# Performance work log

Measured on AMD Instinct MI355X. Metric: run time of the kernel, lower is better.

Reference implementation:

```python
import jax, jax.numpy as jnp
import numpy as np

KAPPA = 0.1          # temperature for sinkhorn routing
SINK_ITERS = 3
SINK_EPS = 1e-6
NORM_EPS = 1e-12     # F.normalize clamp
LOG_EPS = 2.220446049250313e-16  # np.finfo(float).eps
K_TOP = 1


def _l2norm(v, axis=-1):
    n = jnp.sqrt(jnp.sum(v * v, axis=axis, keepdims=True))
    return v / jnp.maximum(n, NORM_EPS)


def _sinkhorn(log_alpha):
    # log_alpha: [K, N]
    L = jnp.exp(log_alpha)
    for _ in range(SINK_ITERS):
        L = L / (jnp.sum(L, axis=1, keepdims=True) + SINK_EPS)
        L = L / (jnp.sum(L, axis=0, keepdims=True) + SINK_EPS)
    return L


def setup_inputs() -> dict:
    key = jax.random.key(0)
    ks = jax.random.split(key, 16)
    dim = 1024
    N = 32768
    lora_dim = [8, 16, 32, 48, 64, 96, 128]
    inp = {
        "x": jax.random.normal(ks[0], (N, dim), dtype=jnp.float32),
        "prototypes": jax.random.normal(ks[1], (7, dim), dtype=jnp.float32),
    }
    for e, d in enumerate(lora_dim):
        # torch Linear weight: [out_features, in_features]
        inp[f"A{e}"] = jax.random.normal(ks[2 + 2 * e], (d, dim), dtype=jnp.float32) * (1.0 / np.sqrt(dim))
        inp[f"B{e}"] = jax.random.normal(ks[3 + 2 * e], (dim, d), dtype=jnp.float32) * (1.0 / np.sqrt(d))
    return inp


def reference(x, prototypes, A0, B0, A1, B1, A2, B2, A3, B3, A4, B4, A5, B5, A6, B6):
    A = [A0, A1, A2, A3, A4, A5, A6]
    B = [B0, B1, B2, B3, B4, B5, B6]
    N = x.shape[0]
    num_experts = len(A)

    # --- sinkhorn routing: gates [N, K] ---
    x_n = _l2norm(x)                       # [N, D]
    p_n = _l2norm(prototypes)              # [K, D]
    sim = jnp.einsum('kd,nd->kn', p_n, x_n)  # [K, N]
    L = _sinkhorn(sim / KAPPA)             # [K, N] doubly-stochastic-ish
    gates_full = L.T                       # [N, K]

    # --- top-k sparsification (k=1) ---
    top_vals, top_idx = jax.lax.top_k(gates_full, K_TOP)  # [N, k]
    gates = jnp.zeros_like(gates_full).at[jnp.arange(N)[:, None], top_idx].set(top_vals)

    # --- per-expert LoRA + weighted log-space combine ---
    # combine: out[b] = log( sum_e gates[b,e] * exp(B_e(A_e(x_b))) ), eps floor
    combined = jnp.zeros_like(x)
    for e in range(num_experts):
        y = jnp.einsum('nr,dr->nd', jnp.einsum('nd,rd->nr', x, A[e]), B[e])  # [N, D]
        combined = combined + gates[:, e:e + 1] * jnp.exp(y)
    combined = jnp.where(combined == 0, LOG_EPS, combined)
    return jnp.log(combined)
```

## Files before the change

### kernel.cpp

```cpp
#include <hip/hip_runtime.h>
#include <math.h>

#define NTOK 32768
#define DIM  1024
#define NE   7
#define TROW 448

#define PN_OFF   0
#define R1_OFF   7168
#define R2_OFF   7176
#define R3_OFF   7184
#define CNT_OFF  7192
#define PR1_OFF  7200
#define PR2_OFF  23584
#define PR3_OFF  24608
#define E0_OFF   25632
#define LG_OFF   287776
#define LIST_OFF 320544
#define A16_OFF  549920
#define B16_OFF  754720
#define TALL_OFF_BYTES 3936384
#define NBLK 2055

#define SEPS 1e-6f

typedef __attribute__((ext_vector_type(8))) short short8v;
typedef __attribute__((ext_vector_type(4))) float f32x4;

constexpr int DV[7]   = {8, 16, 32, 48, 64, 96, 128};
constexpr int DPV[7]  = {32, 32, 32, 64, 64, 96, 128};
constexpr int DAPV[7] = {16, 16, 32, 48, 64, 96, 128};
constexpr int AOV[7]  = {0, 16384, 32768, 65536, 114688, 180224, 278528};
constexpr int BOV[7]  = {0, 32768, 65536, 98304, 163840, 229376, 327680};
constexpr int APRE[7] = {0, 32, 64, 96, 160, 224, 320};
constexpr int TCOL[25] = {0, 32, 64, 80, 96, 112, 128, 160, 176, 192, 208,
                          224, 240, 256, 272, 288, 304,
                          320, 336, 352, 368, 384, 400, 416, 432};

struct ExpPtrs { const float* A[NE]; const float* B[NE]; };

__device__ __forceinline__ short f2bf(float f) {
  union { float f; unsigned u; } v; v.f = f;
  return (short)((v.u + 0x7FFFu + ((v.u >> 16) & 1u)) >> 16);
}

__device__ __forceinline__ float wsum(float v) {
  #pragma unroll
  for (int off = 32; off > 0; off >>= 1) v += __shfl_xor(v, off);
  return v;
}

__device__ __forceinline__ float dot4acc(float4 a, float4 b, float acc) {
  acc = fmaf(a.x, b.x, acc);
  acc = fmaf(a.y, b.y, acc);
  acc = fmaf(a.z, b.z, acc);
  acc = fmaf(a.w, b.w, acc);
  return acc;
}

__device__ __forceinline__ void ecfg(int e, int& d, int& dp, int& dap, int& ao, int& bo) {
  switch (e) {
    case 0: d = 8;   dp = 32;  dap = 16;  ao = 0;      bo = 0;      break;
    case 1: d = 16;  dp = 32;  dap = 16;  ao = 16384;  bo = 32768;  break;
    case 2: d = 32;  dp = 32;  dap = 32;  ao = 32768;  bo = 65536;  break;
    case 3: d = 48;  dp = 64;  dap = 48;  ao = 65536;  bo = 98304;  break;
    case 4: d = 64;  dp = 64;  dap = 64;  ao = 114688; bo = 163840; break;
    case 5: d = 96;  dp = 96;  dap = 96;  ao = 180224; bo = 229376; break;
    default: d = 128; dp = 128; dap = 128; ao = 278528; bo = 327680; break;
  }
}

__global__ __launch_bounds__(256) void k_conv(ExpPtrs p, short* __restrict__ A16,
                                              short* __restrict__ B16,
                                              const float* __restrict__ proto,
                                              float* __restrict__ wsf,
                                              int* __restrict__ counts) {
  const int e = blockIdx.y;
  const int tid = threadIdx.x;
  int d, dp, dap, ao, bo;
  ecfg(e, d, dp, dap, ao, bo);

  if (blockIdx.x == 0) {
    __shared__ float pred[4];
    if (e == 0 && tid < 8) counts[tid] = 0;
    const int w = tid >> 6, lane = tid & 63;
    float v4[4], ss = 0.f;
    #pragma unroll
    for (int i = 0; i < 4; ++i) {
      v4[i] = proto[e * DIM + tid + 256 * i];
      ss = fmaf(v4[i], v4[i], ss);
    }
    ss = wsum(ss);
    if (lane == 0) pred[w] = ss;
    __syncthreads();
    float tot = ((pred[0] + pred[1]) + pred[2]) + pred[3];
    float inv = 1.f / fmaxf(sqrtf(tot), 1e-12f);
    #pragma unroll
    for (int i = 0; i < 4; ++i)
      wsf[PN_OFF + e * DIM + tid + 256 * i] = v4[i] * inv;
  }

  const float* A = p.A[e];
  const float* B = p.B[e];
  short* Ad = A16 + ao;
  short* Bd = B16 + bo;
  const int t0 = blockIdx.x * 256 + tid;
  for (int i = t0; i < dap * DIM; i += 16 * 256) {
    int row = i >> 10;
    Ad[i] = (row < d) ? f2bf(A[i]) : (short)0;
  }
  for (int i = t0; i < DIM * dp; i += 16 * 256) {
    int j = i / dp, r = i - j * dp;
    Bd[i] = (r < d) ? f2bf(B[j * d + r]) : (short)0;
  }
}

__global__ __launch_bounds__(512, 4) void k_simT(const float* __restrict__ x,
                                                 const short* __restrict__ A16,
                                                 const float* __restrict__ wsf,
                                                 float* __restrict__ e0,
                                                 float* __restrict__ pr1,
                                                 short* __restrict__ Tall) {
  __shared__ __align__(16) short As[400 * 40];
  __shared__ float pnS[7][32];
  __shared__ float prS[4][16][8];
  const int tid = threadIdx.x;
  const int n0 = blockIdx.x * 64;

  for (int i = tid; i < 64 * 48; i += 512) {
    int r = i / 48, c = i - r * 48;
    int col = (c < 16) ? (16 + c) : ((c < 32) ? (32 + c) : (112 + c));
    Tall[(size_t)(n0 + r) * TROW + col] = 0;
  }

  const int w = tid >> 6, lane = tid & 63, lo = lane & 15, hi = lane >> 4;
  const int mh = w >> 1, nh = w & 1;
  const int tokBase = n0 + mh * 16;
  const int ts = nh * 12;
  const float* xp = x + (size_t)(tokBase + lo) * DIM + hi * 8;
  const float* PN = wsf + PN_OFF;

  f32x4 acc[13];
  #pragma unroll
  for (int t = 0; t < 13; ++t) acc[t] = (f32x4){0.f, 0.f, 0.f, 0.f};
  float dk[7] = {0.f, 0.f, 0.f, 0.f, 0.f, 0.f, 0.f};
  float xx = 0.f;

  for (int kc = 0; kc < DIM; kc += 32) {
    for (int i = tid; i < 1600; i += 512) {
      int r = i >> 2, q = i & 3;
      *(short8v*)&As[r * 40 + q * 8] =
          *(const short8v*)(A16 + (size_t)r * DIM + kc + q * 8);
    }
    if (tid < 224) pnS[tid >> 5][tid & 31] = PN[(tid >> 5) * DIM + kc + (tid & 31)];
    __syncthreads();

    float4 x0 = *(const float4*)(xp + kc);
    float4 x1 = *(const float4*)(xp + kc + 4);
    short8v af;
    af[0] = f2bf(x0.x); af[1] = f2bf(x0.y); af[2] = f2bf(x0.z); af[3] = f2bf(x0.w);
    af[4] = f2bf(x1.x); af[5] = f2bf(x1.y); af[6] = f2bf(x1.z); af[7] = f2bf(x1.w);

    if (nh == 0) {
      xx = dot4acc(x0, x0, dot4acc(x1, x1, xx));
      #pragma unroll
      for (int k = 0; k < 7; ++k) {
        float4 p0 = *(const float4*)&pnS[k][hi * 8];
        float4 p1 = *(const float4*)&pnS[k][hi * 8 + 4];
        dk[k] = dot4acc(x0, p0, dot4acc(x1, p1, dk[k]));
      }
    }
    #pragma unroll
    for (int tt = 0; tt < 13; ++tt) {
      short8v bf = *(const short8v*)&As[(16 * (ts + tt) + lo) * 40 + hi * 8];
      acc[tt] = __builtin_amdgcn_mfma_f32_16x16x32_bf16(af, bf, acc[tt], 0, 0, 0);
    }
    __syncthreads();
  }

  const int tw = 12 + nh;
  #pragma unroll
  for (int tt = 0; tt < 13; ++tt) {
    if (tt < tw) {
      int col = TCOL[ts + tt] + lo;
      #pragma unroll
      for (int j = 0; j < 4; ++j)
        Tall[(size_t)(tokBase + hi * 4 + j) * TROW + col] = f2bf(acc[tt][j]);
    }
  }

  if (nh == 0) {
    #pragma unroll
    for (int k = 0; k < 7; ++k) {
      dk[k] += __shfl_xor(dk[k], 16);
      dk[k] += __shfl_xor(dk[k], 32);
    }
    xx += __shfl_xor(xx, 16);
    xx += __shfl_xor(xx, 32);
    if (hi == 0) {
      float nrm = fmaxf(sqrtf(xx), 1e-12f);
      int n = tokBase + lo;
      #pragma unroll
      for (int k = 0; k < 7; ++k) {
        float ev = expf((dk[k] / nrm) / 0.1f);
        e0[(size_t)n * 8 + k] = ev;
        prS[mh][lo][k] = ev;
      }
      prS[mh][lo][7] = 0.f;
    }
  }
  __syncthreads();
  if (tid < 8) {
    float s = 0.f;
    for (int m2 = 0; m2 < 4; ++m2)
      for (int l2 = 0; l2 < 16; ++l2) s += prS[m2][l2][tid];
    pr1[blockIdx.x * 8 + tid] = s;
  }
}

#define SUM7(l) (((((((l)[0] + (l)[1]) + (l)[2]) + (l)[3]) + (l)[4]) + (l)[5]) + (l)[6])

template<int DEPTH>
__global__ __launch_bounds__(256) void k_pass(const float* __restrict__ e0,
                                              float* __restrict__ wsf,
                                              const float* __restrict__ src, int nb,
                                              float* __restrict__ prOut,
                                              int* __restrict__ counts,
                                              int* __restrict__ list,
                                              float* __restrict__ lgv) {
  __shared__ float red2[8][33];
  __shared__ float Rcur[8];
  const int tid = threadIdx.x;
  {
    const int k = tid & 7, m = tid >> 3;
    float a = 0.f;
    for (int b = m; b < nb; b += 32) a += src[b * 8 + k];
    red2[k][m] = a;
    __syncthreads();
    if (tid < 8) {
      float s = 0.f;
      for (int mm = 0; mm < 32; ++mm) s += red2[tid][mm];
      Rcur[tid] = s;
      if (blockIdx.x == 0) {
        int roff = (DEPTH == 1) ? R1_OFF : (DEPTH == 2) ? R2_OFF : R3_OFF;
        wsf[roff + tid] = s;
      }
    }
    __syncthreads();
  }

  const int n = blockIdx.x * 256 + tid;
  float4 v0 = *(const float4*)(e0 + (size_t)n * 8);
  float4 v1 = *(const float4*)(e0 + (size_t)n * 8 + 4);
  float l[NE] = {v0.x, v0.y, v0.z, v0.w, v1.x, v1.y, v1.z};
  {
    const float* R1 = (DEPTH == 1) ? Rcur : (wsf + R1_OFF);
    #pragma unroll
    for (int k = 0; k < NE; ++k) l[k] = l[k] / (R1[k] + SEPS);
    float C = SUM7(l);
    #pragma unroll
    for (int k = 0; k < NE; ++k) l[k] = l[k] / (C + SEPS);
  }
  if constexpr (DEPTH >= 2) {
    const float* R2 = (DEPTH == 2) ? Rcur : (wsf + R2_OFF);
    #pragma unroll
    for (int k = 0; k < NE; ++k) l[k] = l[k] / (R2[k] + SEPS);
    float C = SUM7(l);
    #pragma unroll
    for (int k = 0; k < NE; ++k) l[k] = l[k] / (C + SEPS);
  }
  if constexpr (DEPTH >= 3) {
    const float* R3 = Rcur;
    #pragma unroll
    for (int k = 0; k < NE; ++k) l[k] = l[k] / (R3[k] + SEPS);
    float C = SUM7(l);
    #pragma unroll
    for (int k = 0; k < NE; ++k) l[k] = l[k] / (C + SEPS);
  }
  if constexpr (DEPTH == 3) {
    float best = l[0]; int be = 0;
    #pragma unroll
    for (int k = 1; k < NE; ++k) {
      if (l[k] > best) { best = l[k]; be = k; }
    }
    __shared__ int lcnt[8];
    __shared__ int wbase[4][8];
    __shared__ int gbase[8];
    const int w = tid >> 6, lane = tid & 63;
    if (tid < 8) lcnt[tid] = 0;
    __syncthreads();
    int rank = 0;
    #pragma unroll
    for (int k = 0; k < NE; ++k) {
      unsigned long long m = __ballot(be == k);
      if (lane == 0) wbase[w][k] = m ? atomicAdd(&lcnt[k], (int)__popcll(m)) : 0;
      if (be == k) rank = (int)__popcll(m & ((1ull << lane) - 1ull));
    }
    __syncthreads();
    if (tid < 8) gbase[tid] = lcnt[tid] ? atomicAdd(&counts[tid], lcnt[tid]) : 0;
    __syncthreads();
    int pos = gbase[be] + wbase[w][be] + rank;
    list[be * NTOK + pos] = n;
    lgv[n] = logf(best);
  } else {
    __shared__ float red[NE][256];
    #pragma unroll
    for (int k = 0; k < NE; ++k) red[k][tid] = l[k];
    __syncthreads();
    for (int off = 128; off > 0; off >>= 1) {
      if (tid < off) {
        #pragma unroll
        for (int k = 0; k < NE; ++k) red[k][tid] += red[k][tid + off];
      }
      __syncthreads();
    }
    if (tid < NE) prOut[blockIdx.x * 8 + tid] = red[tid][0];
  }
}

__device__ __forceinline__ bool walk(int bid, const int* counts,
                                     int& e, int& tile, int& cnt) {
  int rem = bid; e = 0;
  while (true) {
    cnt = counts[e];
    int tiles = (cnt + 15) >> 4;
    if (rem < tiles) { tile = rem; return true; }
    rem -= tiles;
    if (++e == NE) return false;
  }
}

template<int E>
__device__ void phB_impl(const short* __restrict__ Bp,
                         const short* __restrict__ Tall,
                         const int* __restrict__ list_e,
                         const float* __restrict__ lg,
                         int cnt, int tile, float* __restrict__ out) {
  constexpr int DP = DPV[E];
  constexpr int KS2 = DP / 32;
  const int tid = threadIdx.x;
  const int w = tid >> 6, lane = tid & 63;
  const int lo = lane & 15, hi = lane >> 4;
  const int m0 = tile * 16;

  const int myTok = list_e[min(m0 + lo, cnt - 1)];
  short8v tf[KS2];
  #pragma unroll
  for (int ks = 0; ks < KS2; ++ks)
    tf[ks] = *(const short8v*)(Tall + (size_t)myTok * TROW + APRE[E] + ks * 32 + hi * 8);

  int tok[4]; float lgvr[4];
  #pragma unroll
  for (int j = 0; j < 4; ++j) {
    tok[j] = list_e[min(m0 + hi * 4 + j, cnt - 1)];
    lgvr[j] = lg[tok[j]];
  }

  const short* BpL = Bp + (size_t)(w * 256 + lo) * DP + hi * 8;
  #pragma unroll 1
  for (int nt = 0; nt < 16; ++nt) {
    f32x4 acc = (f32x4){0.f, 0.f, 0.f, 0.f};
    #pragma unroll
    for (int ks = 0; ks < KS2; ++ks) {
      short8v bf = *(const short8v*)(BpL + (size_t)nt * 16 * DP + ks * 32);
      acc = __builtin_amdgcn_mfma_f32_16x16x32_bf16(tf[ks], bf, acc, 0, 0, 0);
    }
    #pragma unroll
    for (int j = 0; j < 4; ++j)
      out[(size_t)tok[j] * DIM + w * 256 + nt * 16 + lo] = acc[j] + lgvr[j];
  }
}

__global__ __launch_bounds__(256, 8) void k_phB(const short* __restrict__ B16,
                                                const short* __restrict__ Tall,
                                                const int* __restrict__ list,
                                                const float* __restrict__ lg,
                                                const int* __restrict__ counts,
                                                float* __restrict__ out) {
  int bid = ((int)blockIdx.x * 1024) % NBLK;
  int e, tile, cnt;
  if (!walk(bid, counts, e, tile, cnt)) return;
  switch (e) {
    case 0: phB_impl<0>(B16 + BOV[0], Tall, list + 0 * NTOK, lg, cnt, tile, out); break;
    case 1: phB_impl<1>(B16 + BOV[1], Tall, list + 1 * NTOK, lg, cnt, tile, out); break;
    case 2: phB_impl<2>(B16 + BOV[2], Tall, list + 2 * NTOK, lg, cnt, tile, out); break;
    case 3: phB_impl<3>(B16 + BOV[3], Tall, list + 3 * NTOK, lg, cnt, tile, out); break;
    case 4: phB_impl<4>(B16 + BOV[4], Tall, list + 4 * NTOK, lg, cnt, tile, out); break;
    case 5: phB_impl<5>(B16 + BOV[5], Tall, list + 5 * NTOK, lg, cnt, tile, out); break;
    default: phB_impl<6>(B16 + BOV[6], Tall, list + 6 * NTOK, lg, cnt, tile, out); break;
  }
}

extern "C" void kernel_launch(void* const* d_in, const int* in_sizes, int n_in,
                              void* d_out, int out_size, void* d_ws, size_t ws_size,
                              hipStream_t stream) {
  const float* x     = (const float*)d_in[0];
  const float* proto = (const float*)d_in[1];
  ExpPtrs p;
  for (int e = 0; e < NE; ++e) {
    p.A[e] = (const float*)d_in[2 + 2 * e];
    p.B[e] = (const float*)d_in[3 + 2 * e];
  }
  float* wsf = (float*)d_ws;
  int*   wsi = (int*)d_ws;
  short* A16 = (short*)(wsf + A16_OFF);
  short* B16 = (short*)(wsf + B16_OFF);
  short* Tall = (short*)((char*)d_ws + TALL_OFF_BYTES);
  float* out = (float*)d_out;

  k_conv<<<dim3(16, NE), 256, 0, stream>>>(p, A16, B16, proto, wsf, wsi + CNT_OFF);
  k_simT<<<512, 512, 0, stream>>>(x, A16, wsf, wsf + E0_OFF, wsf + PR1_OFF, Tall);
  k_pass<1><<<128, 256, 0, stream>>>(wsf + E0_OFF, wsf, wsf + PR1_OFF, 512,
                                     wsf + PR2_OFF, nullptr, nullptr, nullptr);
  k_pass<2><<<128, 256, 0, stream>>>(wsf + E0_OFF, wsf, wsf + PR2_OFF, 128,
                                     wsf + PR3_OFF, nullptr, nullptr, nullptr);
  k_pass<3><<<128, 256, 0, stream>>>(wsf + E0_OFF, wsf, wsf + PR3_OFF, 128,
                                     nullptr, wsi + CNT_OFF, wsi + LIST_OFF, wsf + LG_OFF);
  k_phB<<<NBLK, 256, 0, stream>>>(B16, Tall, wsi + LIST_OFF, wsf + LG_OFF,
                                  wsi + CNT_OFF, out);
}
```

Before: 211.0 us.

## Pre-tile A into LDS-image chunks and stream them with async global-to-LDS loads

The conversion kernel now writes the A weights as per-k-chunk padded LDS images, so k_simT can copy each chunk with global_load_lds directly into shared memory instead of staging through registers. The token tile is halved to 32 with 1024 blocks. The 8 waves split the N-tiles and the prototype dot products four ways, and x and prototype loads are prefetched one chunk ahead. This aims to cut load latency and raise occupancy in the GEMM-plus-similarity pass. In exchange it adds more blocks, more reloads of A per token, and more partial sums for the following reduction pass.

```diff
diff --git a/kernel.cpp b/kernel.cpp
--- a/kernel.cpp
+++ b/kernel.cpp
@@ -17,9 +17,9 @@
 #define E0_OFF   25632
 #define LG_OFF   287776
 #define LIST_OFF 320544
-#define A16_OFF  549920
 #define B16_OFF  754720
-#define TALL_OFF_BYTES 3936384
+#define AIMG_OFF_BYTES 3936384
+#define TALL_OFF_BYTES 4984960
 #define NBLK 2055
 
 #define SEPS 1e-6f
@@ -30,12 +30,14 @@
 constexpr int DV[7]   = {8, 16, 32, 48, 64, 96, 128};
 constexpr int DPV[7]  = {32, 32, 32, 64, 64, 96, 128};
 constexpr int DAPV[7] = {16, 16, 32, 48, 64, 96, 128};
-constexpr int AOV[7]  = {0, 16384, 32768, 65536, 114688, 180224, 278528};
 constexpr int BOV[7]  = {0, 32768, 65536, 98304, 163840, 229376, 327680};
 constexpr int APRE[7] = {0, 32, 64, 96, 160, 224, 320};
+constexpr int RSV[7]  = {0, 16, 32, 64, 112, 176, 272};
 constexpr int TCOL[25] = {0, 32, 64, 80, 96, 112, 128, 160, 176, 192, 208,
                           224, 240, 256, 272, 288, 304,
                           320, 336, 352, 368, 384, 400, 416, 432};
+constexpr int TS4[4] = {0, 7, 13, 19};
+constexpr int TN4[4] = {7, 6, 6, 6};
 
 struct ExpPtrs { const float* A[NE]; const float* B[NE]; };
 
@@ -58,27 +60,20 @@
   return acc;
 }
 
-__device__ __forceinline__ void ecfg(int e, int& d, int& dp, int& dap, int& ao, int& bo) {
-  switch (e) {
-    case 0: d = 8;   dp = 32;  dap = 16;  ao = 0;      bo = 0;      break;
-    case 1: d = 16;  dp = 32;  dap = 16;  ao = 16384;  bo = 32768;  break;
-    case 2: d = 32;  dp = 32;  dap = 32;  ao = 32768;  bo = 65536;  break;
-    case 3: d = 48;  dp = 64;  dap = 48;  ao = 65536;  bo = 98304;  break;
-    case 4: d = 64;  dp = 64;  dap = 64;  ao = 114688; bo = 163840; break;
-    case 5: d = 96;  dp = 96;  dap = 96;  ao = 180224; bo = 229376; break;
-    default: d = 128; dp = 128; dap = 128; ao = 278528; bo = 327680; break;
-  }
-}
-
-__global__ __launch_bounds__(256) void k_conv(ExpPtrs p, short* __restrict__ A16,
+__device__ __forceinline__ void gload_lds16(const void* g, void* l) {
+  __builtin_amdgcn_global_load_lds(
+      (const __attribute__((address_space(1))) unsigned int*)g,
+      (__attribute__((address_space(3))) unsigned int*)l, 16, 0, 0);
+}
+
+__global__ __launch_bounds__(256) void k_conv(ExpPtrs p, short* __restrict__ AIMG,
                                               short* __restrict__ B16,
                                               const float* __restrict__ proto,
                                               float* __restrict__ wsf,
                                               int* __restrict__ counts) {
   const int e = blockIdx.y;
   const int tid = threadIdx.x;
-  int d, dp, dap, ao, bo;
-  ecfg(e, d, dp, dap, ao, bo);
+  const int d = DV[e], dp = DPV[e], dap = DAPV[e], bo = BOV[e], rs = RSV[e];
 
   if (blockIdx.x == 0) {
     __shared__ float pred[4];
@@ -102,86 +97,124 @@
 
   const float* A = p.A[e];
   const float* B = p.B[e];
-  short* Ad = A16 + ao;
+  const int t0 = blockIdx.x * 256 + tid;
+
+  const int tot = dap * 160;
+  for (int i = t0; i < tot; i += 16 * 256) {
+    int lr = i / 160, rem = i - lr * 160;
+    int c = rem / 5, q = rem - c * 5;
+    short8v v = (short8v){0, 0, 0, 0, 0, 0, 0, 0};
+    if (q < 4 && lr < d) {
+      const float* src = A + (size_t)lr * DIM + c * 32 + q * 8;
+      #pragma unroll
+      for (int j = 0; j < 8; ++j) v[j] = f2bf(src[j]);
+    }
+    *(short8v*)&AIMG[c * 16384 + (rs + lr) * 40 + q * 8] = v;
+  }
+  if (e == 0) {
+    for (int i = t0; i < 32 * 48; i += 16 * 256) {
+      int c = i / 48, qq = i - c * 48;
+      *(short8v*)&AIMG[c * 16384 + 16000 + qq * 8] = (short8v){0,0,0,0,0,0,0,0};
+    }
+  }
+
   short* Bd = B16 + bo;
-  const int t0 = blockIdx.x * 256 + tid;
-  for (int i = t0; i < dap * DIM; i += 16 * 256) {
-    int row = i >> 10;
-    Ad[i] = (row < d) ? f2bf(A[i]) : (short)0;
-  }
   for (int i = t0; i < DIM * dp; i += 16 * 256) {
     int j = i / dp, r = i - j * dp;
-    Bd[i] = (r < d) ? f2bf(B[j * d + r]) : (short)0;
-  }
-}
-
-__global__ __launch_bounds__(512, 4) void k_simT(const float* __restrict__ x,
-                                                 const short* __restrict__ A16,
+    Bd[i] = (r < d) ? f2bf(B[(size_t)j * d + r]) : (short)0;
+  }
+}
+
+__global__ __launch_bounds__(512, 6) void k_simT(const float* __restrict__ x,
+                                                 const short* __restrict__ AIMG,
                                                  const float* __restrict__ wsf,
                                                  float* __restrict__ e0,
                                                  float* __restrict__ pr1,
                                                  short* __restrict__ Tall) {
-  __shared__ __align__(16) short As[400 * 40];
+  __shared__ __align__(16) short As[16384];
   __shared__ float pnS[7][32];
-  __shared__ float prS[4][16][8];
+  __shared__ float simS[2][16][8];
   const int tid = threadIdx.x;
-  const int n0 = blockIdx.x * 64;
-
-  for (int i = tid; i < 64 * 48; i += 512) {
+  const int n0 = blockIdx.x * 32;
+  const int w = tid >> 6, lane = tid & 63, lo = lane & 15, hi = lane >> 4;
+  const int mh = w >> 2, nh = w & 3;
+  const int tokBase = n0 + mh * 16;
+  const int ts = TS4[nh], tn = TN4[nh];
+  const int eA = 2 * nh;
+  const bool pnT = tid < 224;
+
+  for (int i = tid; i < 32 * 48; i += 512) {
     int r = i / 48, c = i - r * 48;
     int col = (c < 16) ? (16 + c) : ((c < 32) ? (32 + c) : (112 + c));
     Tall[(size_t)(n0 + r) * TROW + col] = 0;
   }
 
-  const int w = tid >> 6, lane = tid & 63, lo = lane & 15, hi = lane >> 4;
-  const int mh = w >> 1, nh = w & 1;
-  const int tokBase = n0 + mh * 16;
-  const int ts = nh * 12;
-  const float* xp = x + (size_t)(tokBase + lo) * DIM + hi * 8;
+  const float* xp = x + (size_t)(tokBase + lo) * DIM;
   const float* PN = wsf + PN_OFF;
-
-  f32x4 acc[13];
-  #pragma unroll
-  for (int t = 0; t < 13; ++t) acc[t] = (f32x4){0.f, 0.f, 0.f, 0.f};
-  float dk[7] = {0.f, 0.f, 0.f, 0.f, 0.f, 0.f, 0.f};
-  float xx = 0.f;
-
-  for (int kc = 0; kc < DIM; kc += 32) {
-    for (int i = tid; i < 1600; i += 512) {
-      int r = i >> 2, q = i & 3;
-      *(short8v*)&As[r * 40 + q * 8] =
-          *(const short8v*)(A16 + (size_t)r * DIM + kc + q * 8);
-    }
-    if (tid < 224) pnS[tid >> 5][tid & 31] = PN[(tid >> 5) * DIM + kc + (tid & 31)];
-    __syncthreads();
-
-    float4 x0 = *(const float4*)(xp + kc);
-    float4 x1 = *(const float4*)(xp + kc + 4);
+  const char* gA = (const char*)AIMG;
+
+  f32x4 acc[7];
+  #pragma unroll
+  for (int t = 0; t < 7; ++t) acc[t] = (f32x4){0.f, 0.f, 0.f, 0.f};
+  float dkA = 0.f, dkB = 0.f, xx = 0.f;
+
+  #pragma unroll
+  for (int cc = 0; cc < 4; ++cc) {
+    int call = w * 4 + cc;
+    gload_lds16(gA + call * 1024 + lane * 16, (char*)As + call * 1024);
+  }
+  if (pnT) pnS[tid >> 5][tid & 31] = PN[(tid >> 5) * DIM + (tid & 31)];
+  float4 nx0 = *(const float4*)(xp + hi * 8);
+  float4 nx1 = *(const float4*)(xp + hi * 8 + 4);
+  __syncthreads();
+
+  for (int c = 0; c < 32; ++c) {
+    float4 x0 = nx0, x1 = nx1;
+    float pv = 0.f;
+    if (c < 31) {
+      nx0 = *(const float4*)(xp + (c + 1) * 32 + hi * 8);
+      nx1 = *(const float4*)(xp + (c + 1) * 32 + hi * 8 + 4);
+      if (pnT) pv = PN[(tid >> 5) * DIM + (c + 1) * 32 + (tid & 31)];
+    }
     short8v af;
     af[0] = f2bf(x0.x); af[1] = f2bf(x0.y); af[2] = f2bf(x0.z); af[3] = f2bf(x0.w);
     af[4] = f2bf(x1.x); af[5] = f2bf(x1.y); af[6] = f2bf(x1.z); af[7] = f2bf(x1.w);
 
-    if (nh == 0) {
-      xx = dot4acc(x0, x0, dot4acc(x1, x1, xx));
+    {
+      float4 pa0 = *(const float4*)&pnS[eA][hi * 8];
+      float4 pa1 = *(const float4*)&pnS[eA][hi * 8 + 4];
+      dkA = dot4acc(x0, pa0, dot4acc(x1, pa1, dkA));
+      if (nh < 3) {
+        float4 pb0 = *(const float4*)&pnS[eA + 1][hi * 8];
+        float4 pb1 = *(const float4*)&pnS[eA + 1][hi * 8 + 4];
+        dkB = dot4acc(x0, pb0, dot4acc(x1, pb1, dkB));
+      } else {
+        xx = dot4acc(x0, x0, dot4acc(x1, x1, xx));
+      }
+    }
+    #pragma unroll
+    for (int tt = 0; tt < 7; ++tt) {
+      if (tt < tn) {
+        short8v bf = *(const short8v*)&As[(16 * (ts + tt) + lo) * 40 + hi * 8];
+        acc[tt] = __builtin_amdgcn_mfma_f32_16x16x32_bf16(af, bf, acc[tt], 0, 0, 0);
+      }
+    }
+    __syncthreads();
+    if (c < 31) {
       #pragma unroll
-      for (int k = 0; k < 7; ++k) {
-        float4 p0 = *(const float4*)&pnS[k][hi * 8];
-        float4 p1 = *(const float4*)&pnS[k][hi * 8 + 4];
-        dk[k] = dot4acc(x0, p0, dot4acc(x1, p1, dk[k]));
+      for (int cc = 0; cc < 4; ++cc) {
+        int call = w * 4 + cc;
+        gload_lds16(gA + (size_t)(c + 1) * 32768 + call * 1024 + lane * 16,
+                    (char*)As + call * 1024);
       }
-    }
-    #pragma unroll
-    for (int tt = 0; tt < 13; ++tt) {
-      short8v bf = *(const short8v*)&As[(16 * (ts + tt) + lo) * 40 + hi * 8];
-      acc[tt] = __builtin_amdgcn_mfma_f32_16x16x32_bf16(af, bf, acc[tt], 0, 0, 0);
-    }
-    __syncthreads();
-  }
-
-  const int tw = 12 + nh;
-  #pragma unroll
-  for (int tt = 0; tt < 13; ++tt) {
-    if (tt < tw) {
+      if (pnT) pnS[tid >> 5][tid & 31] = pv;
+      __syncthreads();
+    }
+  }
+
+  #pragma unroll
+  for (int tt = 0; tt < 7; ++tt) {
+    if (tt < tn) {
       int col = TCOL[ts + tt] + lo;
       #pragma unroll
       for (int j = 0; j < 4; ++j)
@@ -189,31 +222,34 @@
     }
   }
 
-  if (nh == 0) {
-    #pragma unroll
-    for (int k = 0; k < 7; ++k) {
-      dk[k] += __shfl_xor(dk[k], 16);
-      dk[k] += __shfl_xor(dk[k], 32);
-    }
-    xx += __shfl_xor(xx, 16);
-    xx += __shfl_xor(xx, 32);
-    if (hi == 0) {
-      float nrm = fmaxf(sqrtf(xx), 1e-12f);
-      int n = tokBase + lo;
-      #pragma unroll
-      for (int k = 0; k < 7; ++k) {
-        float ev = expf((dk[k] / nrm) / 0.1f);
-        e0[(size_t)n * 8 + k] = ev;
-        prS[mh][lo][k] = ev;
-      }
-      prS[mh][lo][7] = 0.f;
-    }
+  dkA += __shfl_xor(dkA, 16); dkA += __shfl_xor(dkA, 32);
+  if (nh < 3) { dkB += __shfl_xor(dkB, 16); dkB += __shfl_xor(dkB, 32); }
+  else        { xx  += __shfl_xor(xx, 16);  xx  += __shfl_xor(xx, 32); }
+  if (hi == 0) {
+    simS[mh][lo][eA] = dkA;
+    if (nh < 3) simS[mh][lo][eA + 1] = dkB;
+    else        simS[mh][lo][7] = xx;
+  }
+  __syncthreads();
+  if (tid < 32) {
+    int m2 = tid >> 4, t2 = tid & 15;
+    int n = n0 + m2 * 16 + t2;
+    float xv = simS[m2][t2][7];
+    float nrm = fmaxf(sqrtf(xv), 1e-12f);
+    float ev[8];
+    #pragma unroll
+    for (int k = 0; k < 7; ++k) ev[k] = expf((simS[m2][t2][k] / nrm) / 0.1f);
+    ev[7] = 0.f;
+    *(float4*)&e0[(size_t)n * 8]     = make_float4(ev[0], ev[1], ev[2], ev[3]);
+    *(float4*)&e0[(size_t)n * 8 + 4] = make_float4(ev[4], ev[5], ev[6], ev[7]);
+    #pragma unroll
+    for (int k = 0; k < 8; ++k) simS[m2][t2][k] = ev[k];
   }
   __syncthreads();
   if (tid < 8) {
     float s = 0.f;
-    for (int m2 = 0; m2 < 4; ++m2)
-      for (int l2 = 0; l2 < 16; ++l2) s += prS[m2][l2][tid];
+    for (int m2 = 0; m2 < 2; ++m2)
+      for (int t2 = 0; t2 < 16; ++t2) s += simS[m2][t2][tid];
     pr1[blockIdx.x * 8 + tid] = s;
   }
 }
@@ -401,16 +437,16 @@
     p.A[e] = (const float*)d_in[2 + 2 * e];
     p.B[e] = (const float*)d_in[3 + 2 * e];
   }
-  float* wsf = (float*)d_ws;
-  int*   wsi = (int*)d_ws;
-  short* A16 = (short*)(wsf + A16_OFF);
-  short* B16 = (short*)(wsf + B16_OFF);
+  float* wsf  = (float*)d_ws;
+  int*   wsi  = (int*)d_ws;
+  short* B16  = (short*)(wsf + B16_OFF);
+  short* AIMG = (short*)((char*)d_ws + AIMG_OFF_BYTES);
   short* Tall = (short*)((char*)d_ws + TALL_OFF_BYTES);
-  float* out = (float*)d_out;
-
-  k_conv<<<dim3(16, NE), 256, 0, stream>>>(p, A16, B16, proto, wsf, wsi + CNT_OFF);
-  k_simT<<<512, 512, 0, stream>>>(x, A16, wsf, wsf + E0_OFF, wsf + PR1_OFF, Tall);
-  k_pass<1><<<128, 256, 0, stream>>>(wsf + E0_OFF, wsf, wsf + PR1_OFF, 512,
+  float* out  = (float*)d_out;
+
+  k_conv<<<dim3(16, NE), 256, 0, stream>>>(p, AIMG, B16, proto, wsf, wsi + CNT_OFF);
+  k_simT<<<1024, 512, 0, stream>>>(x, AIMG, wsf, wsf + E0_OFF, wsf + PR1_OFF, Tall);
+  k_pass<1><<<128, 256, 0, stream>>>(wsf + E0_OFF, wsf, wsf + PR1_OFF, 1024,
                                      wsf + PR2_OFF, nullptr, nullptr, nullptr);
   k_pass<2><<<128, 256, 0, stream>>>(wsf + E0_OFF, wsf, wsf + PR2_OFF, 128,
                                      wsf + PR3_OFF, nullptr, nullptr, nullptr);
```

Result: slower. 275.7 us (+30.6%).
